# Kernel tuning notes

Hardware: AMD Instinct MI355X
Metric: run time of the kernel (lower is better)

## Reference

```python
import jax, jax.numpy as jnp
import numpy as np

N = 50000       # nodes
E = 800000      # edges (before self-loops)
NFEAT = 256
NHID = 16       # per-head hidden dim
HEADS = 8
NCLASS = 16
NEG_SLOPE = 0.2  # PyG GATConv default leaky-relu slope


def setup_inputs() -> dict:
    key = jax.random.key(0)
    ks = jax.random.split(key, 10)
    s = 0.05  # weight scale for numerical sanity
    return {
        "x": jax.random.normal(ks[0], (N, NFEAT), jnp.float32),
        "edge_index": jax.random.randint(ks[1], (2, E), 0, N, dtype=jnp.int32),
        "W1": jax.random.normal(ks[2], (NFEAT, HEADS * NHID), jnp.float32) * s,
        "att_src1": jax.random.normal(ks[3], (HEADS, NHID), jnp.float32) * s,
        "att_dst1": jax.random.normal(ks[4], (HEADS, NHID), jnp.float32) * s,
        "b1": jnp.zeros((HEADS * NHID,), jnp.float32),
        "W2": jax.random.normal(ks[5], (HEADS * NHID, NCLASS), jnp.float32) * s,
        "att_src2": jax.random.normal(ks[6], (1, NCLASS), jnp.float32) * s,
        "att_dst2": jax.random.normal(ks[7], (1, NCLASS), jnp.float32) * s,
        "b2": jnp.zeros((NCLASS,), jnp.float32),
    }


def gat_conv(x, edge_index, W, a_src, a_dst, b, heads, out_c, concat):
    """Faithful PyG GATConv (eval mode: dropout off, add_self_loops=True)."""
    n = x.shape[0]
    loop = jnp.arange(n, dtype=edge_index.dtype)
    src = jnp.concatenate([edge_index[0], loop])  # [E+N]
    dst = jnp.concatenate([edge_index[1], loop])  # [E+N]
    h = (x @ W).reshape(n, heads, out_c)          # [N, H, C]
    # per-node attention logits
    alpha_src = jnp.einsum('nhc,hc->nh', h, a_src)  # [N, H]
    alpha_dst = jnp.einsum('nhc,hc->nh', h, a_dst)  # [N, H]
    e = jax.nn.leaky_relu(alpha_src[src] + alpha_dst[dst], NEG_SLOPE)  # [E+N, H]
    # segment softmax over incoming edges of each dst node (self-loop guarantees nonempty)
    m = jax.lax.stop_gradient(jax.ops.segment_max(e, dst, num_segments=n))
    p = jnp.exp(e - m[dst])
    denom = jax.ops.segment_sum(p, dst, num_segments=n)
    a = p / denom[dst]                              # [E+N, H]
    out = jax.ops.segment_sum(a[:, :, None] * h[src], dst, num_segments=n)  # [N, H, C]
    out = out.reshape(n, heads * out_c) if concat else out.mean(axis=1)
    return out + b


def reference(x, edge_index, W1, att_src1, att_dst1, b1, W2, att_src2, att_dst2, b2):
    h1 = jax.nn.elu(gat_conv(x, edge_index, W1, att_src1, att_dst1, b1, HEADS, NHID, True))
    return gat_conv(h1, edge_index, W2, att_src2, att_dst2, b2, 1, NCLASS, False)
```

## Files before the change

kernel.cpp:

```cpp
#include <hip/hip_runtime.h>
#include <hip/hip_bf16.h>

#define NNODES 50000
#define NEDGES 800000
#define NFEATS 256
#define NHID 16
#define HEADS 8
#define NCLS 16
#define NEG_SLOPE 0.2f
#define TOTE (NEDGES + NNODES)
#define RSTRIDE 64
#define NBUCK 196
#define NPB 256
#define BCAP 4864
#define S1_EPT 16

typedef __attribute__((ext_vector_type(8))) short short8;
typedef __attribute__((ext_vector_type(4))) float floatx4;

static __device__ __forceinline__ short f2bf(float f) {
    __hip_bfloat16 b = __float2bfloat16(f);
    return *reinterpret_cast<short*>(&b);
}

#define AS1 __attribute__((address_space(1)))
#define AS3 __attribute__((address_space(3)))

static __device__ __forceinline__ void ld_lds16(const void* g, void* l) {
#if __has_builtin(__builtin_amdgcn_global_load_lds)
    __builtin_amdgcn_global_load_lds((const AS1 void*)g, (AS3 void*)l, 16, 0, 0);
#endif
}


__global__ __launch_bounds__(256) void k_bin(const int* __restrict__ ei,
                                             int* __restrict__ gcnt, int* __restrict__ barr) {
    __shared__ int lcnt[NBUCK], lbase[NBUCK];
    int tid = threadIdx.x;
    if (tid < NBUCK) lcnt[tid] = 0;
    __syncthreads();
    int e0 = blockIdx.x * (256 * S1_EPT) + tid;
    int s[S1_EPT], d[S1_EPT], rk[S1_EPT];
#pragma unroll
    for (int k = 0; k < S1_EPT; k++) {
        int e = e0 + k * 256;
        bool v = e < TOTE;
        int ss = 0, dd = 0;
        if (v) {
            if (e < NEDGES) { ss = ei[e]; dd = ei[NEDGES + e]; }
            else            { ss = e - NEDGES; dd = ss; }
        }
        s[k] = ss; d[k] = dd;
        rk[k] = v ? atomicAdd(&lcnt[dd >> 8], 1) : -1;
    }
    __syncthreads();
    if (tid < NBUCK) lbase[tid] = lcnt[tid] ? atomicAdd(&gcnt[tid], lcnt[tid]) : 0;
    __syncthreads();
#pragma unroll
    for (int k = 0; k < S1_EPT; k++) {
        if (rk[k] >= 0) {
            int b = d[k] >> 8;
            int pos = lbase[b] + rk[k];
            if (pos < BCAP)
                barr[(size_t)b * BCAP + pos] = ((d[k] & 255) << 16) | s[k];
        }
    }
}


__global__ __launch_bounds__(256) void k_csr(const int* __restrict__ gcnt,
                                             const int* __restrict__ barr,
                                             int* __restrict__ cnt, int* __restrict__ csr) {
    __shared__ int lcnt[NPB];
    __shared__ unsigned short lcsr[NPB * 65];
    int b = blockIdx.x, tid = threadIdx.x;
    lcnt[tid] = 0;
    __syncthreads();
    int n = min(gcnt[b], BCAP);
    int nodeBase = b << 8;
    for (int i = tid; i < n; i += 256) {
        int e = barr[(size_t)b * BCAP + i];
        int ln = e >> 16;
        int r = atomicAdd(&lcnt[ln], 1);
        if (r < RSTRIDE) lcsr[ln * 65 + r] = (unsigned short)(e & 0xFFFF);
    }
    __syncthreads();
    int node = nodeBase + tid;
    if (node < NNODES) cnt[node] = min(lcnt[tid], RSTRIDE);
    for (int i = tid; i < NPB * RSTRIDE; i += 256) {
        int ln = i >> 6;
        int nn = nodeBase + ln;
        if (nn < NNODES && (i & 63) < min(lcnt[ln], RSTRIDE))
            csr[(size_t)nodeBase * RSTRIDE + i] = (int)lcsr[ln * 65 + (i & 63)];
    }
}


__global__ void k_prepw(const float* __restrict__ W, const float* __restrict__ a_s,
                        const float* __restrict__ a_d, short* __restrict__ Wsw) {
    int t = blockIdx.x * 256 + threadIdx.x;
    if (t >= 4608) return;
    short8 b;
    if (t < 4096) {
        int kc = t >> 9, nt = (t >> 6) & 7, lane = t & 63;
        int quad = lane >> 4, lo = lane & 15;
#pragma unroll
        for (int j = 0; j < 8; j++)
            b[j] = f2bf(W[(size_t)(kc * 32 + quad * 8 + j) * 128 + nt * 16 + lo]);
    } else {
        int t2 = t - 4096;
        int kc = t2 >> 6, lane = t2 & 63;
        int quad = lane >> 4, lo = lane & 15;
        int h = lo & 7;
        const float* av = (lo < 8) ? (a_s + h * 16) : (a_d + h * 16);
#pragma unroll
        for (int j = 0; j < 8; j++) {
            int k = kc * 32 + quad * 8 + j;
            float acc = 0.f;
#pragma unroll
            for (int c = 0; c < 16; c++) acc += W[(size_t)k * 128 + h * 16 + c] * av[c];
            b[j] = f2bf(acc);
        }
    }
    *(short8*)(Wsw + (size_t)t * 8) = b;
}


__global__ __launch_bounds__(256) void k_gemm1(const float* __restrict__ x,
                                               const short* __restrict__ Wsw,
                                               __hip_bfloat16* __restrict__ h1,
                                               float* __restrict__ as1, float* __restrict__ ad1) {
    __shared__ short bsw[32768];
    int tid  = threadIdx.x;
    int wave = tid >> 6;
    int lane = tid & 63;
    int quad = lane >> 4;
    int lo   = lane & 15;

#if __has_builtin(__builtin_amdgcn_global_load_lds)
    {
        const char* gsrc = (const char*)Wsw + (size_t)wave * 1024 + (size_t)lane * 16;
        char* ldst = (char*)bsw + wave * 1024;
#pragma unroll
        for (int it = 0; it < 16; it++)
            ld_lds16(gsrc + it * 4096, ldst + it * 4096);
    }
#else
    {
        const uint4* g4 = (const uint4*)Wsw;
        uint4* l4 = (uint4*)bsw;
#pragma unroll
        for (int it = 0; it < 16; it++) l4[it * 256 + tid] = g4[it * 256 + tid];
    }
#endif
    short8 wafr[8];
#pragma unroll
    for (int kc = 0; kc < 8; kc++)
        wafr[kc] = *(const short8*)(Wsw + (size_t)(4096 + kc * 64 + lane) * 8);
    __syncthreads();

    int rowBase = blockIdx.x * 128 + wave * 32;
    const float* xa[2];
#pragma unroll
    for (int mt = 0; mt < 2; mt++) {
        int row = rowBase + mt * 16 + lo;
        row = (row < NNODES) ? row : (NNODES - 1);
        xa[mt] = x + (size_t)row * 256 + quad * 8;
    }

    floatx4 acc[2][8], accA[2];
#pragma unroll
    for (int mt = 0; mt < 2; mt++) {
        accA[mt] = (floatx4){0.f, 0.f, 0.f, 0.f};
#pragma unroll
        for (int nt = 0; nt < 8; nt++) acc[mt][nt] = (floatx4){0.f, 0.f, 0.f, 0.f};
    }

    float4 a0[2], a1[2];
#pragma unroll
    for (int mt = 0; mt < 2; mt++) {
        a0[mt] = *(const float4*)(xa[mt]);
        a1[mt] = *(const float4*)(xa[mt] + 4);
    }

    for (int kc = 0; kc < 8; kc++) {
        float4 n0[2], n1[2];
        if (kc < 7) {
#pragma unroll
            for (int mt = 0; mt < 2; mt++) {
                n0[mt] = *(const float4*)(xa[mt] + (kc + 1) * 32);
                n1[mt] = *(const float4*)(xa[mt] + (kc + 1) * 32 + 4);
            }
        }
        short8 afr[2];
#pragma unroll
        for (int mt = 0; mt < 2; mt++) {
            union { short8 s; __hip_bfloat162 h[4]; } u;
            u.h[0] = __float22bfloat162_rn(make_float2(a0[mt].x, a0[mt].y));
            u.h[1] = __float22bfloat162_rn(make_float2(a0[mt].z, a0[mt].w));
            u.h[2] = __float22bfloat162_rn(make_float2(a1[mt].x, a1[mt].y));
            u.h[3] = __float22bfloat162_rn(make_float2(a1[mt].z, a1[mt].w));
            afr[mt] = u.s;
        }
#pragma unroll
        for (int nt = 0; nt < 8; nt++) {
            short8 bfr = *(const short8*)&bsw[((kc * 8 + nt) * 64 + lane) * 8];
            acc[0][nt] = __builtin_amdgcn_mfma_f32_16x16x32_bf16(afr[0], bfr, acc[0][nt], 0, 0, 0);
            acc[1][nt] = __builtin_amdgcn_mfma_f32_16x16x32_bf16(afr[1], bfr, acc[1][nt], 0, 0, 0);
        }
        accA[0] = __builtin_amdgcn_mfma_f32_16x16x32_bf16(afr[0], wafr[kc], accA[0], 0, 0, 0);
        accA[1] = __builtin_amdgcn_mfma_f32_16x16x32_bf16(afr[1], wafr[kc], accA[1], 0, 0, 0);
#pragma unroll
        for (int mt = 0; mt < 2; mt++) { a0[mt] = n0[mt]; a1[mt] = n1[mt]; }
    }

#pragma unroll
    for (int mt = 0; mt < 2; mt++)
#pragma unroll
        for (int nt = 0; nt < 8; nt++)
#pragma unroll
            for (int reg = 0; reg < 4; reg++) {
                int row = rowBase + mt * 16 + quad * 4 + reg;
                int col = nt * 16 + lo;
                if (row < NNODES)
                    h1[(size_t)row * 128 + col] = __float2bfloat16(acc[mt][nt][reg]);
            }
#pragma unroll
    for (int mt = 0; mt < 2; mt++)
#pragma unroll
        for (int reg = 0; reg < 4; reg++) {
            int row = rowBase + mt * 16 + quad * 4 + reg;
            if (row < NNODES) {
                float v = accA[mt][reg];
                if (lo < 8) as1[(size_t)row * 8 + lo] = v;
                else        ad1[(size_t)row * 8 + (lo - 8)] = v;
            }
        }
}


__global__ __launch_bounds__(256) void k_agg1(const int* __restrict__ cnt, const int* __restrict__ csr,
                                              const __hip_bfloat16* __restrict__ h1,
                                              const float* __restrict__ as1, const float* __restrict__ ad1,
                                              const float* __restrict__ b1, __hip_bfloat16* __restrict__ h1act) {
    int wid  = blockIdx.x * 4 + (threadIdx.x >> 6);
    int lane = threadIdx.x & 63;
    int grp  = lane >> 4;
    int cl   = lane & 15;
    int node = wid * 4 + grp;
    int deg  = min(cnt[node], RSTRIDE);
    int head = cl >> 1;
    float adst = ad1[node * 8 + head];
    int rs = node * RSTRIDE;
    int rowv[4];
#pragma unroll
    for (int r = 0; r < 4; r++) rowv[r] = csr[rs + cl + 16 * r];
    int md = deg;
    md = max(md, __shfl_xor(md, 16));
    md = max(md, __shfl_xor(md, 32));

    float acc[8] = {0.f, 0.f, 0.f, 0.f, 0.f, 0.f, 0.f, 0.f};
    float s = 0.f;
#pragma unroll
    for (int r = 0; r < 4; r++) {
        int rbase = r << 4;
        if (rbase >= md) break;
        int lim = min(16, md - rbase);
        for (int i2 = 0; i2 < lim; i2 += 4) {
            float p[4];
            union { short8 v; __hip_bfloat162 h[4]; } u[4];
#pragma unroll
            for (int t = 0; t < 4; t++) {
                int idx = rbase + i2 + t;
                int src = __shfl(rowv[r], (lane & 48) | (idx & 15));
                p[t] = 0.f;
                u[t].v = (short8){0, 0, 0, 0, 0, 0, 0, 0};
                if (idx < deg) {
                    u[t].v = *(const short8*)(h1 + (size_t)src * 128 + cl * 8);
                    float e = as1[src * 8 + head] + adst;
                    e = (e > 0.f) ? e : NEG_SLOPE * e;
                    p[t] = __expf(e);
                }
            }
            s += (p[0] + p[1]) + (p[2] + p[3]);
#pragma unroll
            for (int t = 0; t < 4; t++)
#pragma unroll
                for (int q = 0; q < 4; q++) {
                    float2 f = __bfloat1622float2(u[t].h[q]);
                    acc[q * 2]     = fmaf(p[t], f.x, acc[q * 2]);
                    acc[q * 2 + 1] = fmaf(p[t], f.y, acc[q * 2 + 1]);
                }
        }
    }
    float is = 1.f / s;
    union { short8 v; short us[8]; } pk;
#pragma unroll
    for (int q = 0; q < 8; q++) {
        float v = acc[q] * is + b1[cl * 8 + q];
        v = (v > 0.f) ? v : (__expf(v) - 1.f);
        pk.us[q] = f2bf(v);
    }
    *(short8*)(h1act + (size_t)node * 128 + cl * 8) = pk.v;
}


__global__ __launch_bounds__(256) void k_gemm2(const __hip_bfloat16* __restrict__ h1act,
                                               const float* __restrict__ W2,
                                               const float* __restrict__ a_src,
                                               const float* __restrict__ a_dst,
                                               float* __restrict__ h2,
                                               float* __restrict__ as2, float* __restrict__ ad2) {
    __shared__ float w[128 * 16];
    __shared__ float hr[16][129];
    int tid = threadIdx.x;
    int row0 = blockIdx.x * 16;
    for (int i = tid; i < 2048; i += 256) w[i] = W2[i];
    {
        int r = tid >> 4, k8 = (tid & 15) * 8;
        int gr = row0 + r;
        union { short8 v; __hip_bfloat162 h[4]; } u;
        if (gr < NNODES) u.v = *(const short8*)(h1act + (size_t)gr * 128 + k8);
        else             u.v = (short8){0, 0, 0, 0, 0, 0, 0, 0};
#pragma unroll
        for (int q = 0; q < 4; q++) {
            float2 f = __bfloat1622float2(u.h[q]);
            hr[r][k8 + q * 2]     = f.x;
            hr[r][k8 + q * 2 + 1] = f.y;
        }
    }
    __syncthreads();
    int r = tid >> 4, c = tid & 15;
    float acc = 0.f;
#pragma unroll 8
    for (int k = 0; k < 128; k++) acc += hr[r][k] * w[k * 16 + c];
    int gr = row0 + r;
    if (gr < NNODES) h2[(size_t)gr * 16 + c] = acc;
    float sv = acc * a_src[c];
    float dv = acc * a_dst[c];
#pragma unroll
    for (int o = 1; o <= 8; o <<= 1) {
        sv += __shfl_xor(sv, o);
        dv += __shfl_xor(dv, o);
    }
    if (c == 0 && gr < NNODES) { as2[gr] = sv; ad2[gr] = dv; }
}


__global__ __launch_bounds__(256) void k_agg2(const int* __restrict__ cnt, const int* __restrict__ csr,
                                              const float* __restrict__ h2, const float* __restrict__ as2,
                                              const float* __restrict__ ad2, const float* __restrict__ b2,
                                              float* __restrict__ out) {
    int wid  = blockIdx.x * 4 + (threadIdx.x >> 6);
    int lane = threadIdx.x & 63;
    int grp  = lane >> 4;
    int sub  = lane & 15;
    int slot = sub >> 2;
    int c4   = sub & 3;
    int node = wid * 4 + grp;
    int deg  = min(cnt[node], RSTRIDE);
    float adst = ad2[node];
    int rs = node * RSTRIDE;
    int rowv[4];
#pragma unroll
    for (int r = 0; r < 4; r++) rowv[r] = csr[rs + sub + 16 * r];
    int md = deg;
    md = max(md, __shfl_xor(md, 16));
    md = max(md, __shfl_xor(md, 32));

    float4 acc = make_float4(0.f, 0.f, 0.f, 0.f);
    float s = 0.f;
#pragma unroll
    for (int r = 0; r < 4; r++) {
        int rbase = r << 4;
        if (rbase >= md) break;
        int lim = min(16, md - rbase);
        for (int i2 = 0; i2 < lim; i2 += 8) {
            int ia = rbase + i2 + slot;
            int ib = ia + 4;
            int sa = __shfl(rowv[r], (lane & 48) | ((i2 + slot) & 15));
            int sb = __shfl(rowv[r], (lane & 48) | ((i2 + 4 + slot) & 15));
            float p0 = 0.f, p1 = 0.f;
            float4 r0 = make_float4(0.f, 0.f, 0.f, 0.f);
            float4 r1 = make_float4(0.f, 0.f, 0.f, 0.f);
            if (ia < deg) {
                r0 = *(const float4*)(h2 + (size_t)sa * 16 + c4 * 4);
                float e = as2[sa] + adst;
                e = (e > 0.f) ? e : NEG_SLOPE * e;
                p0 = __expf(e);
            }
            if (ib < deg) {
                r1 = *(const float4*)(h2 + (size_t)sb * 16 + c4 * 4);
                float e = as2[sb] + adst;
                e = (e > 0.f) ? e : NEG_SLOPE * e;
                p1 = __expf(e);
            }
            s += p0 + p1;
            acc.x = fmaf(p0, r0.x, fmaf(p1, r1.x, acc.x));
            acc.y = fmaf(p0, r0.y, fmaf(p1, r1.y, acc.y));
            acc.z = fmaf(p0, r0.z, fmaf(p1, r1.z, acc.z));
            acc.w = fmaf(p0, r0.w, fmaf(p1, r1.w, acc.w));
        }
    }
#pragma unroll
    for (int o = 4; o <= 8; o <<= 1) {
        acc.x += __shfl_xor(acc.x, o);
        acc.y += __shfl_xor(acc.y, o);
        acc.z += __shfl_xor(acc.z, o);
        acc.w += __shfl_xor(acc.w, o);
        s += __shfl_xor(s, o);
    }
    if (slot == 0) {
        float is = 1.f / s;
        float4 o4;
        o4.x = acc.x * is + b2[c4 * 4 + 0];
        o4.y = acc.y * is + b2[c4 * 4 + 1];
        o4.z = acc.z * is + b2[c4 * 4 + 2];
        o4.w = acc.w * is + b2[c4 * 4 + 3];
        *(float4*)(out + (size_t)node * 16 + c4 * 4) = o4;
    }
}


extern "C" void kernel_launch(void* const* d_in, const int* in_sizes, int n_in,
                              void* d_out, int out_size, void* d_ws, size_t ws_size,
                              hipStream_t stream) {
    const float* x    = (const float*)d_in[0];
    const int*   ei   = (const int*)d_in[1];
    const float* W1   = (const float*)d_in[2];
    const float* a_s1 = (const float*)d_in[3];
    const float* a_d1 = (const float*)d_in[4];
    const float* b1   = (const float*)d_in[5];
    const float* W2   = (const float*)d_in[6];
    const float* a_s2 = (const float*)d_in[7];
    const float* a_d2 = (const float*)d_in[8];
    const float* b2   = (const float*)d_in[9];
    float* out = (float*)d_out;

    char* p = (char*)d_ws;
    auto alloc = [&](size_t bytes) -> char* {
        char* q = p;
        p += (bytes + 255) & ~(size_t)255;
        return q;
    };
    int*  gcnt = (int*)alloc(NBUCK * 4);
    int*  barr = (int*)alloc((size_t)NBUCK * BCAP * 4);
    int*  cnt  = (int*)alloc((size_t)NNODES * 4);
    int*  csr  = (int*)alloc((size_t)NNODES * RSTRIDE * 4);
    short* Wsw = (short*)alloc((size_t)36864 * 2);
    __hip_bfloat16* h1 = (__hip_bfloat16*)alloc((size_t)NNODES * 128 * 2);
    float* as1 = (float*)alloc((size_t)NNODES * 8 * 4);
    float* ad1 = (float*)alloc((size_t)NNODES * 8 * 4);
    __hip_bfloat16* h1act = (__hip_bfloat16*)alloc((size_t)NNODES * 128 * 2);
    float* h2  = (float*)as1;
    float* as2 = (float*)barr;
    float* ad2 = (float*)barr + NNODES;

    hipMemsetAsync(gcnt, 0, NBUCK * 4, stream);
    hipLaunchKernelGGL(k_bin,   dim3((TOTE + 4095) / 4096), dim3(256), 0, stream, ei, gcnt, barr);
    hipLaunchKernelGGL(k_csr,   dim3(NBUCK), dim3(256), 0, stream, gcnt, barr, cnt, csr);
    hipLaunchKernelGGL(k_prepw, dim3(18), dim3(256), 0, stream, W1, a_s1, a_d1, Wsw);
    hipLaunchKernelGGL(k_gemm1, dim3((NNODES + 127) / 128), dim3(256), 0, stream, x, Wsw, h1, as1, ad1);
    hipLaunchKernelGGL(k_agg1,  dim3(NNODES / 16), dim3(256), 0, stream, cnt, csr, h1, as1, ad1, b1, h1act);
    hipLaunchKernelGGL(k_gemm2, dim3((NNODES + 15) / 16), dim3(256), 0, stream, h1act, W2, a_s2, a_d2, h2, as2, ad2);
    hipLaunchKernelGGL(k_agg2,  dim3(NNODES / 16), dim3(256), 0, stream, cnt, csr, h2, as2, ad2, b2, out);
}
```

Measured before the change: 220.8 us.

## Fuse layer-2 linear projection into layer-1 aggregation kernel

Merges the second-layer GEMM (h1act @ W2 plus the attention logits) into the first aggregation kernel. Activated rows stay in shared memory and are multiplied by a transposed W2 tile, so the bf16 h1act intermediate is never written or re-read and one launch is removed. Blocks grow to 512 threads covering 32 nodes, with clamped node indices, and the edge loop now processes 8 neighbors per iteration instead of 4. In exchange it uses more shared memory, adds a block barrier, and raises register pressure, which may lower occupancy in the gather-bound aggregation.

```diff
diff --git a/kernel.cpp b/kernel.cpp
--- a/kernel.cpp
+++ b/kernel.cpp
@@ -239,19 +239,29 @@
 }
 
 
-__global__ __launch_bounds__(256) void k_agg1(const int* __restrict__ cnt, const int* __restrict__ csr,
+__global__ __launch_bounds__(512) void k_agg1(const int* __restrict__ cnt, const int* __restrict__ csr,
                                               const __hip_bfloat16* __restrict__ h1,
                                               const float* __restrict__ as1, const float* __restrict__ ad1,
-                                              const float* __restrict__ b1, __hip_bfloat16* __restrict__ h1act) {
-    int wid  = blockIdx.x * 4 + (threadIdx.x >> 6);
-    int lane = threadIdx.x & 63;
-    int grp  = lane >> 4;
+                                              const float* __restrict__ b1,
+                                              const float* __restrict__ W2,
+                                              const float* __restrict__ a_s2, const float* __restrict__ a_d2,
+                                              float* __restrict__ h2,
+                                              float* __restrict__ as2, float* __restrict__ ad2) {
+    __shared__ float hl[32][128];
+    __shared__ float w2t[16][132];
+    int tid = threadIdx.x;
+    for (int i = tid; i < 2048; i += 512)
+        w2t[i >> 7][i & 127] = W2[(i & 127) * 16 + (i >> 7)];
+
+    int lane = tid & 63;
     int cl   = lane & 15;
-    int node = wid * 4 + grp;
-    int deg  = min(cnt[node], RSTRIDE);
+    int ln   = tid >> 4;
+    int node = blockIdx.x * 32 + ln;
+    int nodeC = min(node, NNODES - 1);
+    int deg  = min(cnt[nodeC], RSTRIDE);
     int head = cl >> 1;
-    float adst = ad1[node * 8 + head];
-    int rs = node * RSTRIDE;
+    float adst = ad1[nodeC * 8 + head];
+    int rs = nodeC * RSTRIDE;
     int rowv[4];
 #pragma unroll
     for (int r = 0; r < 4; r++) rowv[r] = csr[rs + cl + 16 * r];
@@ -266,13 +276,13 @@
         int rbase = r << 4;
         if (rbase >= md) break;
         int lim = min(16, md - rbase);
-        for (int i2 = 0; i2 < lim; i2 += 4) {
-            float p[4];
-            union { short8 v; __hip_bfloat162 h[4]; } u[4];
-#pragma unroll
-            for (int t = 0; t < 4; t++) {
+        for (int i2 = 0; i2 < lim; i2 += 8) {
+            float p[8];
+            union { short8 v; __hip_bfloat162 h[4]; } u[8];
+#pragma unroll
+            for (int t = 0; t < 8; t++) {
                 int idx = rbase + i2 + t;
-                int src = __shfl(rowv[r], (lane & 48) | (idx & 15));
+                int src = __shfl(rowv[r], (lane & 48) | ((i2 + t) & 15));
                 p[t] = 0.f;
                 u[t].v = (short8){0, 0, 0, 0, 0, 0, 0, 0};
                 if (idx < deg) {
@@ -282,9 +292,10 @@
                     p[t] = __expf(e);
                 }
             }
-            s += (p[0] + p[1]) + (p[2] + p[3]);
-#pragma unroll
-            for (int t = 0; t < 4; t++)
+#pragma unroll
+            for (int t = 0; t < 8; t++) s += p[t];
+#pragma unroll
+            for (int t = 0; t < 8; t++)
 #pragma unroll
                 for (int q = 0; q < 4; q++) {
                     float2 f = __bfloat1622float2(u[t].h[q]);
@@ -293,57 +304,36 @@
                 }
         }
     }
-    float is = 1.f / s;
-    union { short8 v; short us[8]; } pk;
-#pragma unroll
-    for (int q = 0; q < 8; q++) {
-        float v = acc[q] * is + b1[cl * 8 + q];
-        v = (v > 0.f) ? v : (__expf(v) - 1.f);
-        pk.us[q] = f2bf(v);
-    }
-    *(short8*)(h1act + (size_t)node * 128 + cl * 8) = pk.v;
-}
-
-
-__global__ __launch_bounds__(256) void k_gemm2(const __hip_bfloat16* __restrict__ h1act,
-                                               const float* __restrict__ W2,
-                                               const float* __restrict__ a_src,
-                                               const float* __restrict__ a_dst,
-                                               float* __restrict__ h2,
-                                               float* __restrict__ as2, float* __restrict__ ad2) {
-    __shared__ float w[128 * 16];
-    __shared__ float hr[16][129];
-    int tid = threadIdx.x;
-    int row0 = blockIdx.x * 16;
-    for (int i = tid; i < 2048; i += 256) w[i] = W2[i];
     {
-        int r = tid >> 4, k8 = (tid & 15) * 8;
-        int gr = row0 + r;
-        union { short8 v; __hip_bfloat162 h[4]; } u;
-        if (gr < NNODES) u.v = *(const short8*)(h1act + (size_t)gr * 128 + k8);
-        else             u.v = (short8){0, 0, 0, 0, 0, 0, 0, 0};
-#pragma unroll
-        for (int q = 0; q < 4; q++) {
-            float2 f = __bfloat1622float2(u.h[q]);
-            hr[r][k8 + q * 2]     = f.x;
-            hr[r][k8 + q * 2 + 1] = f.y;
-        }
-    }
-    __syncthreads();
-    int r = tid >> 4, c = tid & 15;
-    float acc = 0.f;
-#pragma unroll 8
-    for (int k = 0; k < 128; k++) acc += hr[r][k] * w[k * 16 + c];
-    int gr = row0 + r;
-    if (gr < NNODES) h2[(size_t)gr * 16 + c] = acc;
-    float sv = acc * a_src[c];
-    float dv = acc * a_dst[c];
+        float is = 1.f / s;
+        float o[8];
+#pragma unroll
+        for (int q = 0; q < 8; q++) {
+            float v = acc[q] * is + b1[cl * 8 + q];
+            o[q] = (v > 0.f) ? v : (__expf(v) - 1.f);
+        }
+        *(float4*)&hl[ln][cl * 8]     = make_float4(o[0], o[1], o[2], o[3]);
+        *(float4*)&hl[ln][cl * 8 + 4] = make_float4(o[4], o[5], o[6], o[7]);
+    }
+    __syncthreads();
+    float h2v = 0.f;
+#pragma unroll
+    for (int k4 = 0; k4 < 128; k4 += 4) {
+        float4 hv = *(const float4*)&hl[ln][k4];
+        float4 wv = *(const float4*)&w2t[cl][k4];
+        h2v += hv.x * wv.x + hv.y * wv.y + hv.z * wv.z + hv.w * wv.w;
+    }
+    float sv = h2v * a_s2[cl];
+    float dv = h2v * a_d2[cl];
 #pragma unroll
     for (int o = 1; o <= 8; o <<= 1) {
         sv += __shfl_xor(sv, o);
         dv += __shfl_xor(dv, o);
     }
-    if (c == 0 && gr < NNODES) { as2[gr] = sv; ad2[gr] = dv; }
+    if (node < NNODES) {
+        h2[(size_t)node * 16 + cl] = h2v;
+        if (cl == 0) { as2[node] = sv; ad2[node] = dv; }
+    }
 }
 
 
@@ -451,17 +441,16 @@
     __hip_bfloat16* h1 = (__hip_bfloat16*)alloc((size_t)NNODES * 128 * 2);
     float* as1 = (float*)alloc((size_t)NNODES * 8 * 4);
     float* ad1 = (float*)alloc((size_t)NNODES * 8 * 4);
-    __hip_bfloat16* h1act = (__hip_bfloat16*)alloc((size_t)NNODES * 128 * 2);
-    float* h2  = (float*)as1;
     float* as2 = (float*)barr;
     float* ad2 = (float*)barr + NNODES;
+    float* h2  = (float*)barr + 2 * NNODES;
 
     hipMemsetAsync(gcnt, 0, NBUCK * 4, stream);
     hipLaunchKernelGGL(k_bin,   dim3((TOTE + 4095) / 4096), dim3(256), 0, stream, ei, gcnt, barr);
     hipLaunchKernelGGL(k_csr,   dim3(NBUCK), dim3(256), 0, stream, gcnt, barr, cnt, csr);
     hipLaunchKernelGGL(k_prepw, dim3(18), dim3(256), 0, stream, W1, a_s1, a_d1, Wsw);
     hipLaunchKernelGGL(k_gemm1, dim3((NNODES + 127) / 128), dim3(256), 0, stream, x, Wsw, h1, as1, ad1);
-    hipLaunchKernelGGL(k_agg1,  dim3(NNODES / 16), dim3(256), 0, stream, cnt, csr, h1, as1, ad1, b1, h1act);
-    hipLaunchKernelGGL(k_gemm2, dim3((NNODES + 15) / 16), dim3(256), 0, stream, h1act, W2, a_s2, a_d2, h2, as2, ad2);
+    hipLaunchKernelGGL(k_agg1,  dim3((NNODES + 31) / 32), dim3(512), 0, stream,
+                       cnt, csr, h1, as1, ad1, b1, W2, a_s2, a_d2, h2, as2, ad2);
     hipLaunchKernelGGL(k_agg2,  dim3(NNODES / 16), dim3(256), 0, stream, cnt, csr, h2, as2, ad2, b2, out);
 }
```

New measurement: 222.6 us. Within noise of the previous version (+0.8%).
